# Kernel optimization log

Measured on AMD Instinct MI355X. Metric: run time of the kernel, lower is better.

Reference implementation:

```python
import jax, jax.numpy as jnp
import numpy as np

BITS = 4
MAXQ = (1 << BITS) - 1          # 15
PACK = 32 // BITS               # 8 values per int32
GROUP_SIZE = 128
IN_F, OUT_F = 4096, 11008


def setup_inputs() -> dict:
    key = jax.random.key(0)
    k1, k2, k3, k4, k5 = jax.random.split(key, 5)
    x = jax.random.normal(k1, (4, 2048, IN_F), dtype=jnp.float32)
    scales = jax.random.uniform(k2, (IN_F // GROUP_SIZE, OUT_F), dtype=jnp.float32) * 0.01
    bias = jax.random.normal(k3, (OUT_F,), dtype=jnp.float32)
    qweight = jax.random.randint(k4, (IN_F // PACK, OUT_F), 0, 2147483647, dtype=jnp.int32)
    qzeros = jax.random.randint(k5, (IN_F // GROUP_SIZE, OUT_F // PACK), 0, 2147483647, dtype=jnp.int32)
    return {"x": x, "scales": scales, "bias": bias, "qweight": qweight, "qzeros": qzeros}


def _dequant(qweight, qzeros, scales):
    shifts = (jnp.arange(PACK, dtype=jnp.int32) * BITS)
    # unpack along dim0: each int32 row holds PACK consecutive input rows
    w = ((qweight[:, None, :] >> shifts[None, :, None]) & MAXQ)  # [IN_F/PACK, PACK, OUT_F]
    w = w.reshape(IN_F, OUT_F).astype(scales.dtype)
    # unpack along dim1: each int32 col holds PACK consecutive output cols
    z = ((qzeros[:, :, None] >> shifts[None, None, :]) & MAXQ)   # [G, OUT_F/PACK, PACK]
    z = z.reshape(qzeros.shape[0], OUT_F).astype(scales.dtype)
    # per-group affine dequant: (w - zero) * scale
    weight = ((w.reshape(-1, GROUP_SIZE, OUT_F) - z[:, None, :]) * scales[:, None, :])
    return weight.reshape(IN_F, OUT_F)


def reference(x, scales, bias, qweight, qzeros):
    weight = _dequant(qweight, qzeros, scales).astype(x.dtype)
    out = jnp.matmul(x, weight)  # [B, S, OUT_F]
    return out + bias.astype(out.dtype)
```

## Files before the change

kernel.cpp:

```cpp
#include <hip/hip_runtime.h>
#include <hip/hip_bf16.h>
#include <stdint.h>

#define IN_F   4096
#define OUT_F  11008
#define M_TOT  8192
#define ZCOLS  (OUT_F / 8)
#define KK_ROWS (IN_F / 8)

#define BM 256
#define BN 256
#define BK 64
#define NT (IN_F / BK)
#define GRID_M (M_TOT / BM)
#define GRID_N (OUT_F / BN)
#define NWG (GRID_M * GRID_N)
#define CPX (NWG / 8)

typedef __attribute__((ext_vector_type(8))) short  bf16x8;
typedef __attribute__((ext_vector_type(8))) ushort ushort8;
typedef __attribute__((ext_vector_type(4))) float  f32x4;

__device__ __forceinline__ ushort f2bf(float f) {
    __hip_bfloat16 h = __float2bfloat16(f);
    return *reinterpret_cast<ushort*>(&h);
}

__global__ void convert_x(const float4* __restrict__ x, ushort8* __restrict__ xb) {
    size_t t = (size_t)blockIdx.x * 256 + threadIdx.x;
    float4 a = x[2 * t];
    float4 b = x[2 * t + 1];
    ushort8 o;
    o[0] = f2bf(a.x); o[1] = f2bf(a.y); o[2] = f2bf(a.z); o[3] = f2bf(a.w);
    o[4] = f2bf(b.x); o[5] = f2bf(b.y); o[6] = f2bf(b.z); o[7] = f2bf(b.w);
    xb[t] = o;
}

__global__ __launch_bounds__(256)
void dequant_w(const int* __restrict__ qw, const int* __restrict__ qz,
               const float* __restrict__ sc, ushort* __restrict__ wt) {
    __shared__ ushort tile[64 * 512];

    const int bid = blockIdx.x;
    const int n0  = (bid % (OUT_F / 64)) * 64;
    const int kk0 = (bid / (OUT_F / 64)) * 64;
    const int tid = threadIdx.x;
    const int nl  = tid & 63;
    const int kr  = tid >> 6;

    const int ng  = n0 + nl;
    const int zsh = (ng & 7) * 4;
    const int zc  = ng >> 3;

#pragma unroll
    for (int p = 0; p < 16; ++p) {
        const int kk  = p * 4 + kr;
        const int gkk = kk0 + kk;
        const int g   = gkk >> 4;
        const int w   = qw[gkk * OUT_F + ng];
        const int z   = (qz[g * ZCOLS + zc] >> zsh) & 15;
        const float s = sc[g * OUT_F + ng];
        ushort8 r;
#pragma unroll
        for (int i = 0; i < 8; ++i) {
            int q = (w >> (4 * i)) & 15;
            r[i] = f2bf((float)(q - z) * s);
        }
        *(ushort8*)&tile[nl * 512 + ((kk * 8) ^ (nl << 3 & 511))] = r;
    }
    __syncthreads();

    const int c   = tid & 63;
    const int nr4 = tid >> 6;
#pragma unroll
    for (int p = 0; p < 16; ++p) {
        const int nr = p * 4 + nr4;
        ushort8 v = *(const ushort8*)&tile[nr * 512 + ((c * 8) ^ (nr << 3 & 511))];
        *(ushort8*)&wt[(size_t)(n0 + nr) * IN_F + kk0 * 8 + c * 8] = v;
    }
}

__global__ __launch_bounds__(512, 2)
void gemm_bf16(const ushort* __restrict__ A, const ushort* __restrict__ Bt,
               const float* __restrict__ bias, float* __restrict__ C) {
    __shared__ ushort smem[8][8192];

    const int tid  = threadIdx.x;
    const int wave = tid >> 6;
    const int lane = tid & 63;

    const int bid = blockIdx.x;
    const int swz = (bid & 7) * CPX + (bid >> 3);
    const int bm0 = (swz / GRID_N) * BM;
    const int bn0 = (swz % GRID_N) * BN;

    const int wm = wave >> 2;
    const int wn = wave & 3;
    const int lm = lane & 15;
    const int lq = lane >> 4;

    const int sr   = lane >> 3;
    const int scol = 8 * ((lane & 7) ^ sr);

    const ushort* aSrc[2][2];
    const ushort* bSrc[2][2];
#pragma unroll
    for (int j = 0; j < 2; ++j) {
        const int r = wave * 16 + j * 8 + sr;
#pragma unroll
        for (int h = 0; h < 2; ++h) {
            aSrc[h][j] = A  + (size_t)(bm0 + ((r >> 6) << 7) + h * 64 + (r & 63)) * IN_F + scol;
            bSrc[h][j] = Bt + (size_t)(bn0 + ((r >> 5) << 6) + h * 32 + (r & 31)) * IN_F + scol;
        }
    }

    const int cswz0 = (lq * 8)      ^ ((lm & 7) << 3);
    const int cswz1 = (32 + lq * 8) ^ ((lm & 7) << 3);

    f32x4  acc[8][4] = {};
    bf16x8 af[4][2];
    bf16x8 ball[2][2][2];

#define STAGE_A(buf, mh, kt) do {                                                        \
    _Pragma("unroll")                                                                    \
    for (int j_ = 0; j_ < 2; ++j_)                                                       \
        __builtin_amdgcn_global_load_lds(                                                \
            (const __attribute__((address_space(1))) void*)(aSrc[mh][j_] + (size_t)(kt) * BK), \
            (__attribute__((address_space(3))) void*)(&smem[(buf) * 4 + (mh)][(wave * 2 + j_) * 512]), \
            16, 0, 0);                                                                   \
} while (0)

#define STAGE_B(buf, nh, kt) do {                                                        \
    _Pragma("unroll")                                                                    \
    for (int j_ = 0; j_ < 2; ++j_)                                                       \
        __builtin_amdgcn_global_load_lds(                                                \
            (const __attribute__((address_space(1))) void*)(bSrc[nh][j_] + (size_t)(kt) * BK), \
            (__attribute__((address_space(3))) void*)(&smem[(buf) * 4 + 2 + (nh)][(wave * 2 + j_) * 512]), \
            16, 0, 0);                                                                   \
} while (0)

#define LDA(buf, mh) do {                                                                \
    const ushort* ab_ = &smem[(buf) * 4 + (mh)][wm * 4096 + lm * 64];                    \
    _Pragma("unroll")                                                                    \
    for (int i_ = 0; i_ < 4; ++i_) {                                                     \
        af[i_][0] = *(const bf16x8*)(ab_ + i_ * 1024 + cswz0);                           \
        af[i_][1] = *(const bf16x8*)(ab_ + i_ * 1024 + cswz1);                           \
    }                                                                                    \
} while (0)

#define LDB2(buf) do {                                                                   \
    _Pragma("unroll")                                                                    \
    for (int nh_ = 0; nh_ < 2; ++nh_) {                                                  \
        const ushort* bb_ = &smem[(buf) * 4 + 2 + nh_][wn * 2048 + lm * 64];             \
        _Pragma("unroll")                                                                \
        for (int j_ = 0; j_ < 2; ++j_) {                                                 \
            ball[nh_][j_][0] = *(const bf16x8*)(bb_ + j_ * 1024 + cswz0);                \
            ball[nh_][j_][1] = *(const bf16x8*)(bb_ + j_ * 1024 + cswz1);                \
        }                                                                                \
    }                                                                                    \
} while (0)

#define MFMA_Q(mh, nh) do {                                                              \
    __builtin_amdgcn_s_setprio(1);                                                       \
    _Pragma("unroll")                                                                    \
    for (int i_ = 0; i_ < 4; ++i_)                                                       \
        _Pragma("unroll")                                                                \
        for (int j_ = 0; j_ < 2; ++j_)                                                   \
            _Pragma("unroll")                                                            \
            for (int k_ = 0; k_ < 2; ++k_)                                               \
                acc[(mh) * 4 + i_][(nh) * 2 + j_] = __builtin_amdgcn_mfma_f32_16x16x32_bf16( \
                    af[i_][k_], ball[nh][j_][k_], acc[(mh) * 4 + i_][(nh) * 2 + j_], 0, 0, 0); \
    __builtin_amdgcn_s_setprio(0);                                                       \
} while (0)

#define BAR()   asm volatile("s_barrier" ::: "memory")
#define LGKM0() asm volatile("s_waitcnt lgkmcnt(0)" ::: "memory")
#define VM(n)   asm volatile("s_waitcnt vmcnt(" #n ")" ::: "memory")

    STAGE_A(0, 0, 0);
    STAGE_B(0, 1, 0);
    STAGE_A(0, 1, 0);
    STAGE_B(0, 0, 0);
    STAGE_A(1, 0, 1);
    STAGE_B(1, 1, 1);
    STAGE_A(1, 1, 1);
    VM(6);
    BAR();

#pragma unroll 1
    for (int it = 0; it < NT / 2; ++it) {
        const int t1 = 2 * it + 1;
        int s2 = 2 * it + 2; if (s2 > NT - 1) s2 = NT - 1;
        int s3 = 2 * it + 3; if (s3 > NT - 1) s3 = NT - 1;

        LDA(0, 0); LDB2(0);
        STAGE_B(1, 0, t1);
        BAR(); LGKM0();
        MFMA_Q(0, 0);
        BAR();

        STAGE_A(0, 0, s2);
        BAR(); LGKM0();
        MFMA_Q(0, 1);
        BAR();

        LDA(0, 1);
        STAGE_B(0, 1, s2);
        BAR(); LGKM0();
        MFMA_Q(1, 1);
        BAR();

        STAGE_A(0, 1, s2);
        BAR(); LGKM0();
        MFMA_Q(1, 0);
        VM(6);
        BAR();

        LDA(1, 0); LDB2(1);
        STAGE_B(0, 0, s2);
        BAR(); LGKM0();
        MFMA_Q(0, 0);
        BAR();

        STAGE_A(1, 0, s3);
        BAR(); LGKM0();
        MFMA_Q(0, 1);
        BAR();

        LDA(1, 1);
        STAGE_B(1, 1, s3);
        BAR(); LGKM0();
        MFMA_Q(1, 1);
        BAR();

        STAGE_A(1, 1, s3);
        BAR(); LGKM0();
        MFMA_Q(1, 0);
        VM(6);
        BAR();
    }

    VM(0);

    const int cm0 = bm0 + wm * 128 + lq * 4;
    const int cn0 = bn0 + wn * 64 + lm;
#pragma unroll
    for (int nt2 = 0; nt2 < 4; ++nt2) {
        const int n = cn0 + nt2 * 16;
        const float bv = bias[n];
#pragma unroll
        for (int mt = 0; mt < 8; ++mt) {
            float* out = C + (size_t)(cm0 + mt * 16) * OUT_F + n;
#pragma unroll
            for (int r = 0; r < 4; ++r)
                out[(size_t)r * OUT_F] = acc[mt][nt2][r] + bv;
        }
    }

#undef STAGE_A
#undef STAGE_B
#undef LDA
#undef LDB2
#undef MFMA_Q
#undef BAR
#undef LGKM0
#undef VM
}

extern "C" void kernel_launch(void* const* d_in, const int* in_sizes, int n_in,
                              void* d_out, int out_size, void* d_ws, size_t ws_size,
                              hipStream_t stream) {
    const float* x       = (const float*)d_in[0];
    const float* scales  = (const float*)d_in[1];
    const float* bias    = (const float*)d_in[2];
    const int*   qweight = (const int*)d_in[3];
    const int*   qzeros  = (const int*)d_in[4];
    float* out = (float*)d_out;

    ushort* xb = (ushort*)d_ws;
    ushort* wt = (ushort*)((char*)d_ws + (size_t)M_TOT * IN_F * 2);

    convert_x<<<(M_TOT * IN_F / 8) / 256, 256, 0, stream>>>((const float4*)x, (ushort8*)xb);
    dequant_w<<<(OUT_F / 64) * (KK_ROWS / 64), 256, 0, stream>>>(qweight, qzeros, scales, wt);
    gemm_bf16<<<NWG, 512, 0, stream>>>(xb, wt, bias, out);
}
```

Before: 1.074 ms.

## Make bf16 GEMM persistent with cross-tile prefetch of next tile's K stages

The GEMM becomes a persistent kernel with 256 workgroups, each looping over output tiles in steps of 32 along the swizzled order. The final K step of each tile already stages the first K slices of the next tile, so loads overlap the epilogue and no new workgroup has to refill the pipeline. The MFMA issue order is also reordered so the k-half is the outermost loop. In exchange, only one workgroup runs per CU where launch bounds allowed two. Workgroups also get either 5 or 6 tiles, so the tail imbalance remains.

Result: slower. 1.131 ms (+5.2%).

```diff
diff --git a/kernel.cpp b/kernel.cpp
--- a/kernel.cpp
+++ b/kernel.cpp
@@ -16,6 +16,7 @@
 #define GRID_N (OUT_F / BN)
 #define NWG (GRID_M * GRID_N)
 #define CPX (NWG / 8)
+#define PBLK 256
 
 typedef __attribute__((ext_vector_type(8))) short  bf16x8;
 typedef __attribute__((ext_vector_type(8))) ushort ushort8;
@@ -89,10 +90,12 @@
     const int wave = tid >> 6;
     const int lane = tid & 63;
 
-    const int bid = blockIdx.x;
-    const int swz = (bid & 7) * CPX + (bid >> 3);
-    const int bm0 = (swz / GRID_N) * BM;
-    const int bn0 = (swz % GRID_N) * BN;
+    const int bid    = blockIdx.x;
+    const int ntiles = (NWG - bid + PBLK - 1) >> 8;
+
+    int swz = (bid & 7) * CPX + (bid >> 3);
+    int bm0 = (swz / GRID_N) * BM;
+    int bn0 = (swz % GRID_N) * BN;
 
     const int wm = wave >> 2;
     const int wn = wave & 3;
@@ -102,39 +105,42 @@
     const int sr   = lane >> 3;
     const int scol = 8 * ((lane & 7) ^ sr);
 
-    const ushort* aSrc[2][2];
-    const ushort* bSrc[2][2];
-#pragma unroll
-    for (int j = 0; j < 2; ++j) {
-        const int r = wave * 16 + j * 8 + sr;
-#pragma unroll
-        for (int h = 0; h < 2; ++h) {
-            aSrc[h][j] = A  + (size_t)(bm0 + ((r >> 6) << 7) + h * 64 + (r & 63)) * IN_F + scol;
-            bSrc[h][j] = Bt + (size_t)(bn0 + ((r >> 5) << 6) + h * 32 + (r & 31)) * IN_F + scol;
-        }
-    }
-
     const int cswz0 = (lq * 8)      ^ ((lm & 7) << 3);
     const int cswz1 = (32 + lq * 8) ^ ((lm & 7) << 3);
 
-    f32x4  acc[8][4] = {};
+    const ushort* aCur[2][2]; const ushort* bCur[2][2];
+    const ushort* aNxt[2][2]; const ushort* bNxt[2][2];
+
+#define MKPTR(bm_, bn_, AS, BS) do {                                                     \
+    _Pragma("unroll")                                                                    \
+    for (int j_ = 0; j_ < 2; ++j_) {                                                     \
+        const int r_ = wave * 16 + j_ * 8 + sr;                                          \
+        _Pragma("unroll")                                                                \
+        for (int h_ = 0; h_ < 2; ++h_) {                                                 \
+            AS[h_][j_] = A  + (size_t)((bm_) + ((r_ >> 6) << 7) + h_ * 64 + (r_ & 63)) * IN_F + scol; \
+            BS[h_][j_] = Bt + (size_t)((bn_) + ((r_ >> 5) << 6) + h_ * 32 + (r_ & 31)) * IN_F + scol; \
+        }                                                                                \
+    }                                                                                    \
+} while (0)
+
+    f32x4  acc[8][4];
     bf16x8 af[4][2];
     bf16x8 ball[2][2][2];
 
-#define STAGE_A(buf, mh, kt) do {                                                        \
+#define STAGE_A(P, buf, mh, kt) do {                                                     \
     _Pragma("unroll")                                                                    \
     for (int j_ = 0; j_ < 2; ++j_)                                                       \
         __builtin_amdgcn_global_load_lds(                                                \
-            (const __attribute__((address_space(1))) void*)(aSrc[mh][j_] + (size_t)(kt) * BK), \
+            (const __attribute__((address_space(1))) void*)(P[mh][j_] + (size_t)(kt) * BK), \
             (__attribute__((address_space(3))) void*)(&smem[(buf) * 4 + (mh)][(wave * 2 + j_) * 512]), \
             16, 0, 0);                                                                   \
 } while (0)
 
-#define STAGE_B(buf, nh, kt) do {                                                        \
+#define STAGE_B(P, buf, nh, kt) do {                                                     \
     _Pragma("unroll")                                                                    \
     for (int j_ = 0; j_ < 2; ++j_)                                                       \
         __builtin_amdgcn_global_load_lds(                                                \
-            (const __attribute__((address_space(1))) void*)(bSrc[nh][j_] + (size_t)(kt) * BK), \
+            (const __attribute__((address_space(1))) void*)(P[nh][j_] + (size_t)(kt) * BK), \
             (__attribute__((address_space(3))) void*)(&smem[(buf) * 4 + 2 + (nh)][(wave * 2 + j_) * 512]), \
             16, 0, 0);                                                                   \
 } while (0)
@@ -163,11 +169,11 @@
 #define MFMA_Q(mh, nh) do {                                                              \
     __builtin_amdgcn_s_setprio(1);                                                       \
     _Pragma("unroll")                                                                    \
-    for (int i_ = 0; i_ < 4; ++i_)                                                       \
+    for (int k_ = 0; k_ < 2; ++k_)                                                       \
         _Pragma("unroll")                                                                \
-        for (int j_ = 0; j_ < 2; ++j_)                                                   \
+        for (int i_ = 0; i_ < 4; ++i_)                                                   \
             _Pragma("unroll")                                                            \
-            for (int k_ = 0; k_ < 2; ++k_)                                               \
+            for (int j_ = 0; j_ < 2; ++j_)                                               \
                 acc[(mh) * 4 + i_][(nh) * 2 + j_] = __builtin_amdgcn_mfma_f32_16x16x32_bf16( \
                     af[i_][k_], ball[nh][j_][k_], acc[(mh) * 4 + i_][(nh) * 2 + j_], 0, 0, 0); \
     __builtin_amdgcn_s_setprio(0);                                                       \
@@ -177,86 +183,111 @@
 #define LGKM0() asm volatile("s_waitcnt lgkmcnt(0)" ::: "memory")
 #define VM(n)   asm volatile("s_waitcnt vmcnt(" #n ")" ::: "memory")
 
-    STAGE_A(0, 0, 0);
-    STAGE_B(0, 1, 0);
-    STAGE_A(0, 1, 0);
-    STAGE_B(0, 0, 0);
-    STAGE_A(1, 0, 1);
-    STAGE_B(1, 1, 1);
-    STAGE_A(1, 1, 1);
+#define KSTEP(PA, PB, kt1, k2, k3) do {                                                  \
+                    \
+    LDA(0, 0); LDB2(0);                                                                  \
+    STAGE_B(bCur, 1, 0, kt1);                                                            \
+    BAR(); LGKM0();                                                                      \
+    MFMA_Q(0, 0);                                                                        \
+    BAR();                                                                               \
+                                                 \
+    STAGE_A(PA, 0, 0, k2);                                                               \
+    BAR(); LGKM0();                                                                      \
+    MFMA_Q(0, 1);                                                                        \
+    BAR();                                                                               \
+                                                   \
+    LDA(0, 1);                                                                           \
+    STAGE_B(PB, 0, 1, k2);                                                               \
+    BAR(); LGKM0();                                                                      \
+    MFMA_Q(1, 1);                                                                        \
+    BAR();                                                                               \
+                                  \
+    STAGE_A(PA, 0, 1, k2);                                                               \
+    BAR(); LGKM0();                                                                      \
+    MFMA_Q(1, 0);                                                                        \
+    VM(6);                                                                               \
+    BAR();                                                                               \
+                             \
+    LDA(1, 0); LDB2(1);                                                                  \
+    STAGE_B(PB, 0, 0, k2);                                                               \
+    BAR(); LGKM0();                                                                      \
+    MFMA_Q(0, 0);                                                                        \
+    BAR();                                                                               \
+                                                 \
+    STAGE_A(PA, 1, 0, k3);                                                               \
+    BAR(); LGKM0();                                                                      \
+    MFMA_Q(0, 1);                                                                        \
+    BAR();                                                                               \
+                                                   \
+    LDA(1, 1);                                                                           \
+    STAGE_B(PB, 1, 1, k3);                                                               \
+    BAR(); LGKM0();                                                                      \
+    MFMA_Q(1, 1);                                                                        \
+    BAR();                                                                               \
+                                  \
+    STAGE_A(PA, 1, 1, k3);                                                               \
+    BAR(); LGKM0();                                                                      \
+    MFMA_Q(1, 0);                                                                        \
+    VM(6);                                                                               \
+    BAR();                                                                               \
+} while (0)
+
+    MKPTR(bm0, bn0, aCur, bCur);
+    STAGE_A(aCur, 0, 0, 0);
+    STAGE_B(bCur, 0, 1, 0);
+    STAGE_A(aCur, 0, 1, 0);
+    STAGE_B(bCur, 0, 0, 0);
+    STAGE_A(aCur, 1, 0, 1);
+    STAGE_B(bCur, 1, 1, 1);
+    STAGE_A(aCur, 1, 1, 1);
     VM(6);
     BAR();
 
 #pragma unroll 1
-    for (int it = 0; it < NT / 2; ++it) {
-        const int t1 = 2 * it + 1;
-        int s2 = 2 * it + 2; if (s2 > NT - 1) s2 = NT - 1;
-        int s3 = 2 * it + 3; if (s3 > NT - 1) s3 = NT - 1;
-
-        LDA(0, 0); LDB2(0);
-        STAGE_B(1, 0, t1);
-        BAR(); LGKM0();
-        MFMA_Q(0, 0);
-        BAR();
-
-        STAGE_A(0, 0, s2);
-        BAR(); LGKM0();
-        MFMA_Q(0, 1);
-        BAR();
-
-        LDA(0, 1);
-        STAGE_B(0, 1, s2);
-        BAR(); LGKM0();
-        MFMA_Q(1, 1);
-        BAR();
-
-        STAGE_A(0, 1, s2);
-        BAR(); LGKM0();
-        MFMA_Q(1, 0);
-        VM(6);
-        BAR();
-
-        LDA(1, 0); LDB2(1);
-        STAGE_B(0, 0, s2);
-        BAR(); LGKM0();
-        MFMA_Q(0, 0);
-        BAR();
-
-        STAGE_A(1, 0, s3);
-        BAR(); LGKM0();
-        MFMA_Q(0, 1);
-        BAR();
-
-        LDA(1, 1);
-        STAGE_B(1, 1, s3);
-        BAR(); LGKM0();
-        MFMA_Q(1, 1);
-        BAR();
-
-        STAGE_A(1, 1, s3);
-        BAR(); LGKM0();
-        MFMA_Q(1, 0);
-        VM(6);
-        BAR();
+    for (int t = 0; t < ntiles; ++t) {
+        const int swzN = swz + 32;
+        int bm0N = bm0, bn0N = bn0;
+        if (t != ntiles - 1) { bm0N = (swzN / GRID_N) * BM; bn0N = (swzN % GRID_N) * BN; }
+        MKPTR(bm0N, bn0N, aNxt, bNxt);
+
+#pragma unroll
+        for (int i = 0; i < 8; ++i)
+#pragma unroll
+            for (int j = 0; j < 4; ++j)
+                acc[i][j] = (f32x4){0.f, 0.f, 0.f, 0.f};
+
+#pragma unroll 1
+        for (int it = 0; it < 31; ++it) {
+            KSTEP(aCur, bCur, 2 * it + 1, 2 * it + 2, 2 * it + 3);
+        }
+        KSTEP(aNxt, bNxt, 63, 0, 1);
+
+        const int cm0 = bm0 + wm * 128 + lq * 4;
+        const int cn0 = bn0 + wn * 64 + lm;
+#pragma unroll
+        for (int nt2 = 0; nt2 < 4; ++nt2) {
+            const int n = cn0 + nt2 * 16;
+            const float bv = bias[n];
+#pragma unroll
+            for (int mt = 0; mt < 8; ++mt) {
+                float* out = C + (size_t)(cm0 + mt * 16) * OUT_F + n;
+#pragma unroll
+                for (int r = 0; r < 4; ++r)
+                    out[(size_t)r * OUT_F] = acc[mt][nt2][r] + bv;
+            }
+        }
+
+        swz = swzN; bm0 = bm0N; bn0 = bn0N;
+#pragma unroll
+        for (int j = 0; j < 2; ++j)
+#pragma unroll
+            for (int h = 0; h < 2; ++h) {
+                aCur[h][j] = aNxt[h][j];
+                bCur[h][j] = bNxt[h][j];
+            }
     }
 
-    VM(0);
-
-    const int cm0 = bm0 + wm * 128 + lq * 4;
-    const int cn0 = bn0 + wn * 64 + lm;
-#pragma unroll
-    for (int nt2 = 0; nt2 < 4; ++nt2) {
-        const int n = cn0 + nt2 * 16;
-        const float bv = bias[n];
-#pragma unroll
-        for (int mt = 0; mt < 8; ++mt) {
-            float* out = C + (size_t)(cm0 + mt * 16) * OUT_F + n;
-#pragma unroll
-            for (int r = 0; r < 4; ++r)
-                out[(size_t)r * OUT_F] = acc[mt][nt2][r] + bv;
-        }
-    }
-
+#undef MKPTR
 #undef STAGE_A
 #undef STAGE_B
 #undef LDA
@@ -265,6 +296,7 @@
 #undef BAR
 #undef LGKM0
 #undef VM
+#undef KSTEP
 }
 
 extern "C" void kernel_launch(void* const* d_in, const int* in_sizes, int n_in,
@@ -282,5 +314,5 @@
 
     convert_x<<<(M_TOT * IN_F / 8) / 256, 256, 0, stream>>>((const float4*)x, (ushort8*)xb);
     dequant_w<<<(OUT_F / 64) * (KK_ROWS / 64), 256, 0, stream>>>(qweight, qzeros, scales, wt);
-    gemm_bf16<<<NWG, 512, 0, stream>>>(xb, wt, bias, out);
-}
+    gemm_bf16<<<PBLK, 512, 0, stream>>>(xb, wt, bias, out);
+}
```
